# Optimization experiments

Measured on AMD Instinct MI355X. Metric: run time of the kernel, lower is better.

## Reference

```python
import jax, jax.numpy as jnp
import numpy as np

N_NODES = 50000
N_EDGES = 625000
HIDDEN = 128
N_TYPES = 4


def setup_inputs() -> dict:
    key = jax.random.key(0)
    ks = jax.random.split(key, 10)
    s = 1.0 / np.sqrt(HIDDEN)
    return {
        "node_states": jax.random.normal(ks[0], (N_NODES, HIDDEN), dtype=jnp.float32),
        "edge_index": jax.random.randint(ks[1], (2, N_EDGES), 0, N_NODES, dtype=jnp.int64),
        "edge_type": jax.random.randint(ks[2], (N_EDGES,), 0, N_TYPES, dtype=jnp.int64),
        # per-edge-type Linear(hidden, hidden): weight [T, d, d] (torch: y = x @ W.T + b)
        "edge_W": jax.random.uniform(ks[3], (N_TYPES, HIDDEN, HIDDEN), jnp.float32, -s, s),
        "edge_b": jax.random.uniform(ks[4], (N_TYPES, HIDDEN), jnp.float32, -s, s),
        # GRUCell params (torch layout: [3d, d] for r|z|n gates)
        "w_ih": jax.random.uniform(ks[5], (3 * HIDDEN, HIDDEN), jnp.float32, -s, s),
        "w_hh": jax.random.uniform(ks[6], (3 * HIDDEN, HIDDEN), jnp.float32, -s, s),
        "b_ih": jax.random.uniform(ks[7], (3 * HIDDEN,), jnp.float32, -s, s),
        "b_hh": jax.random.uniform(ks[8], (3 * HIDDEN,), jnp.float32, -s, s),
    }


def reference(node_states, edge_index, edge_type, edge_W, edge_b, w_ih, w_hh, b_ih, b_hh):
    num_nodes = node_states.shape[0]
    src, dst = edge_index[0], edge_index[1]
    x_src = node_states[src]  # [E, d] gather of source states

    # per-edge-type linear; small fixed loop over edge types, masked accumulate
    msgs = jnp.zeros_like(x_src)
    for t in range(edge_W.shape[0]):
        m_t = x_src @ edge_W[t].T + edge_b[t]  # [E, d]
        msgs = msgs + jnp.where((edge_type == t)[:, None], m_t, 0.0)

    # scatter-sum messages into destination nodes
    agg = jax.ops.segment_sum(msgs, dst, num_segments=num_nodes)  # [N, d]

    # GRUCell(agg, node_states) — torch semantics
    gi = agg @ w_ih.T + b_ih          # [N, 3d]
    gh = node_states @ w_hh.T + b_hh  # [N, 3d]
    i_r, i_z, i_n = jnp.split(gi, 3, axis=1)
    h_r, h_z, h_n = jnp.split(gh, 3, axis=1)
    r = jax.nn.sigmoid(i_r + h_r)
    z = jax.nn.sigmoid(i_z + h_z)
    n = jnp.tanh(i_n + r * h_n)
    return (1.0 - z) * n + z * node_states
```

## Files before the change

### kernel.cpp

```cpp
#include <hip/hip_runtime.h>


typedef __attribute__((ext_vector_type(8))) short short8;
typedef __attribute__((ext_vector_type(4))) float floatx4;

#define HID 128
#define NTY 4

__device__ __forceinline__ unsigned short f2bf(float f) {
    unsigned int u = __float_as_uint(f);
    unsigned int r = (u + 0x7fffu + ((u >> 16) & 1u)) >> 16;
    return (unsigned short)r;
}
__device__ __forceinline__ float bf2f(unsigned int lo16) {
    return __uint_as_float(lo16 << 16);
}


__global__ void prep_kernel(const float* __restrict__ h, unsigned short* __restrict__ hbf,
                            const float* __restrict__ W, unsigned short* __restrict__ Wc,
                            const float* __restrict__ w_ih, const float* __restrict__ w_hh,
                            unsigned short* __restrict__ Wg, int* __restrict__ deg4,
                            int total4, int nb_cvt, int N4) {
    int b = blockIdx.x, tt = threadIdx.x;
    if (b < nb_cvt) {
        int i = b * 256 + tt;
        if (i < total4) {
            float4 v = ((const float4*)h)[i];
            uint2 o;
            o.x = (unsigned int)f2bf(v.x) | ((unsigned int)f2bf(v.y) << 16);
            o.y = (unsigned int)f2bf(v.z) | ((unsigned int)f2bf(v.w) << 16);
            ((uint2*)hbf)[i] = o;
        }
    } else if (b < nb_cvt + 256) {
        int idx = (b - nb_cvt) * 256 + tt;
        int j = idx >> 9, rem = idx & 511;
        int t = rem >> 7, k = rem & 127;
        Wc[idx] = f2bf(W[(t * HID + j) * HID + k]);
    } else if (b < nb_cvt + 768) {
        int idx = (b - nb_cvt - 256) * 256 + tt;
        int row = idx >> 8, k = idx & 255;
        int j = row >> 2, g = row & 3;
        float v = 0.0f;
        if (g == 0) v = (k < 128) ? w_ih[j * 128 + k]         : w_hh[j * 128 + (k - 128)];
        else if (g == 1) v = (k < 128) ? w_ih[(128 + j) * 128 + k] : w_hh[(128 + j) * 128 + (k - 128)];
        else if (g == 2) v = (k < 128) ? w_ih[(256 + j) * 128 + k] : 0.0f;
        else             v = (k < 128) ? 0.0f : w_hh[(256 + j) * 128 + (k - 128)];
        Wg[idx] = f2bf(v);
    } else {
        int i = (b - nb_cvt - 768) * 256 + tt;
        if (i < N4) deg4[i] = 0;
    }
}


__global__ void hist4_kernel(const int* __restrict__ dst, const int* __restrict__ ety,
                             int* __restrict__ deg4, int E) {
    int e = blockIdx.x * blockDim.x + threadIdx.x;
    if (e < E) atomicAdd(&deg4[dst[e] * 4 + ety[e]], 1);
}

__global__ void scan_blocks4_kernel(const int* __restrict__ deg, int* __restrict__ rowptr,
                                    int* __restrict__ blocksum, int N4) {
    __shared__ int s[256];
    int t = threadIdx.x;
    int base = blockIdx.x * 1024 + t * 4;
    int v0 = 0, v1 = 0, v2 = 0, v3 = 0;
    if (base + 3 < N4) {
        v0 = deg[base]; v1 = deg[base + 1]; v2 = deg[base + 2]; v3 = deg[base + 3];
    } else {
        if (base < N4) v0 = deg[base];
        if (base + 1 < N4) v1 = deg[base + 1];
        if (base + 2 < N4) v2 = deg[base + 2];
    }
    int sum = v0 + v1 + v2 + v3;
    s[t] = sum;
    __syncthreads();
#pragma unroll
    for (int off = 1; off < 256; off <<= 1) {
        int x = (t >= off) ? s[t - off] : 0;
        __syncthreads();
        s[t] += x;
        __syncthreads();
    }
    int ex = s[t] - sum;
    if (base < N4) rowptr[base] = ex;
    if (base + 1 < N4) rowptr[base + 1] = ex + v0;
    if (base + 2 < N4) rowptr[base + 2] = ex + v0 + v1;
    if (base + 3 < N4) rowptr[base + 3] = ex + v0 + v1 + v2;
    if (t == 255) blocksum[blockIdx.x] = s[255];
}

__global__ void scan_top_kernel(const int* __restrict__ blocksum, int* __restrict__ blockoff, int nb) {
    __shared__ int s[256];
    int t = threadIdx.x;
    int v = (t < nb) ? blocksum[t] : 0;
    s[t] = v;
    __syncthreads();
#pragma unroll
    for (int off = 1; off < 256; off <<= 1) {
        int x = (t >= off) ? s[t - off] : 0;
        __syncthreads();
        s[t] += x;
        __syncthreads();
    }
    if (t < nb) blockoff[t] = s[t] - v;
}

__global__ void finalize4_kernel(int* __restrict__ rowptr, const int* __restrict__ blockoff,
                                 int* __restrict__ cursor, int N4, int E) {
    int i = blockIdx.x * blockDim.x + threadIdx.x;
    if (i >= N4) return;
    int r = rowptr[i] + blockoff[i >> 10];
    rowptr[i] = r;
    cursor[i] = r;
    if (i == 0) rowptr[N4] = E;
}

__global__ void fill4_kernel(const int* __restrict__ src, const int* __restrict__ dst,
                             const int* __restrict__ ety, int* __restrict__ cursor,
                             int* __restrict__ csr, int E) {
    int e = blockIdx.x * blockDim.x + threadIdx.x;
    if (e >= E) return;
    int pos = atomicAdd(&cursor[dst[e] * 4 + ety[e]], 1);
    csr[pos] = src[e];
}


__global__ void gather_s_kernel(const int* __restrict__ rowptr4, const int* __restrict__ csr,
                                const unsigned int* __restrict__ hbu,
                                float4* __restrict__ cnt4, unsigned int* __restrict__ Su, int N) {
    int w = blockIdx.x * (blockDim.x >> 6) + (threadIdx.x >> 6);
    if (w >= N) return;
    int lane = threadIdx.x & 63;
    int b0 = rowptr4[w * 4];
    int b1 = rowptr4[w * 4 + 1];
    int b2 = rowptr4[w * 4 + 2];
    int b3 = rowptr4[w * 4 + 3];
    int b4 = rowptr4[w * 4 + 4];

    float s0 = 0.f, s1 = 0.f;
    float sn0[4], sn1[4];
    int e = b0;
#pragma unroll
    for (int t = 0; t < 4; ++t) {
        int bend = (t == 0) ? b1 : (t == 1) ? b2 : (t == 2) ? b3 : b4;
        for (; e + 8 <= bend; e += 8) {
            int p[8];
            unsigned int u[8];
#pragma unroll
            for (int i = 0; i < 8; ++i) p[i] = csr[e + i];
#pragma unroll
            for (int i = 0; i < 8; ++i) u[i] = hbu[(size_t)p[i] * 64 + lane];
#pragma unroll
            for (int i = 0; i < 8; ++i) {
                s0 += bf2f(u[i] & 0xffffu);
                s1 += bf2f(u[i] >> 16);
            }
        }
        for (; e + 4 <= bend; e += 4) {
            int p[4];
            unsigned int u[4];
#pragma unroll
            for (int i = 0; i < 4; ++i) p[i] = csr[e + i];
#pragma unroll
            for (int i = 0; i < 4; ++i) u[i] = hbu[(size_t)p[i] * 64 + lane];
#pragma unroll
            for (int i = 0; i < 4; ++i) {
                s0 += bf2f(u[i] & 0xffffu);
                s1 += bf2f(u[i] >> 16);
            }
        }
        for (; e < bend; ++e) {
            unsigned int u = hbu[(size_t)csr[e] * 64 + lane];
            s0 += bf2f(u & 0xffffu);
            s1 += bf2f(u >> 16);
        }
        sn0[t] = s0;
        sn1[t] = s1;
    }
    float p0 = 0.f, p1 = 0.f;
    size_t base = (size_t)w * 256 + lane;
#pragma unroll
    for (int t = 0; t < 4; ++t) {
        float a0 = sn0[t] - p0, a1 = sn1[t] - p1;
        p0 = sn0[t]; p1 = sn1[t];
        Su[base + t * 64] = (unsigned int)f2bf(a0) | ((unsigned int)f2bf(a1) << 16);
    }
    if (lane == 0)
        cnt4[w] = make_float4((float)(b1 - b0), (float)(b2 - b1),
                              (float)(b3 - b2), (float)(b4 - b3));
}


__global__ __launch_bounds__(256) void agg_gemm(const unsigned short* __restrict__ S,
                                                const unsigned short* __restrict__ Wc,
                                                const float4* __restrict__ cnt4,
                                                const float* __restrict__ eb,
                                                unsigned short* __restrict__ aggbf, int M) {
    __shared__ __align__(16) unsigned short Ss[128][136];
    const int tid = threadIdx.x;
    const int m0 = blockIdx.x * 128;
    const int lane = tid & 63, wave = tid >> 6;
    const int wm = wave >> 1, wn = wave & 1;
    const int lm = lane & 15, quad = lane >> 4;

    floatx4 acc[4][4];
#pragma unroll
    for (int a = 0; a < 4; ++a)
#pragma unroll
        for (int b = 0; b < 4; ++b) acc[a][b] = (floatx4){0.f, 0.f, 0.f, 0.f};

    for (int c = 0; c < 4; ++c) {
        {
            int rr = tid >> 4;
            int cc = (tid & 15) * 8;
#pragma unroll
            for (int p = 0; p < 8; ++p) {
                int r = rr + p * 16;
                int gm = m0 + r;
                uint4 v = {0u, 0u, 0u, 0u};
                if (gm < M) v = *(const uint4*)(S + (size_t)gm * 512 + c * 128 + cc);
                *(uint4*)&Ss[r][cc] = v;
            }
        }
        __syncthreads();
#pragma unroll
        for (int s = 0; s < 4; ++s) {
            short8 af[4], bfr[4];
#pragma unroll
            for (int mi = 0; mi < 4; ++mi)
                af[mi] = *(const short8*)&Ss[wm * 64 + mi * 16 + lm][s * 32 + quad * 8];
#pragma unroll
            for (int ni = 0; ni < 4; ++ni) {
                int j = wn * 64 + ni * 16 + lm;
                bfr[ni] = *(const short8*)(Wc + (size_t)j * 512 + c * 128 + s * 32 + quad * 8);
            }
#pragma unroll
            for (int mi = 0; mi < 4; ++mi)
#pragma unroll
                for (int ni = 0; ni < 4; ++ni)
                    acc[mi][ni] = __builtin_amdgcn_mfma_f32_16x16x32_bf16(af[mi], bfr[ni], acc[mi][ni], 0, 0, 0);
        }
        __syncthreads();
    }
#pragma unroll
    for (int mi = 0; mi < 4; ++mi) {
        int row_b = wm * 64 + mi * 16 + quad * 4;
#pragma unroll
        for (int r = 0; r < 4; ++r) {
            int lrow = row_b + r;
            int node = m0 + lrow;
            float4 c4 = (node < M) ? cnt4[node] : make_float4(0.f, 0.f, 0.f, 0.f);
#pragma unroll
            for (int ni = 0; ni < 4; ++ni) {
                int j = wn * 64 + ni * 16 + lm;
                float v = acc[mi][ni][r];
                v += c4.x * eb[j] + c4.y * eb[HID + j] + c4.z * eb[2 * HID + j] + c4.w * eb[3 * HID + j];
                Ss[lrow][j] = f2bf(v);
            }
        }
    }
    __syncthreads();
    {
        int row = tid >> 1;
        int halfc = (tid & 1) * 64;
        int node = m0 + row;
        if (node < M) {
#pragma unroll
            for (int i = 0; i < 8; ++i)
                *(uint4*)(aggbf + (size_t)node * HID + halfc + i * 8) = *(const uint4*)&Ss[row][halfc + i * 8];
        }
    }
}


__global__ __launch_bounds__(256) void gemm_gru(const unsigned short* __restrict__ Wg,
                                                const unsigned short* __restrict__ aggbf,
                                                const unsigned short* __restrict__ hbf,
                                                const float* __restrict__ b_ih,
                                                const float* __restrict__ b_hh,
                                                float* __restrict__ out, int M) {
    __shared__ __align__(16) unsigned short Xs[64][136];
    __shared__ __align__(16) float Outs[64][68];
    const int tid = threadIdx.x;
    const int n0 = blockIdx.x * 64;
    const int gh = blockIdx.y;
    const int lane = tid & 63, w = tid >> 6;
    const int lm = lane & 15, quad = lane >> 4;

    floatx4 acc[4][4];
#pragma unroll
    for (int a = 0; a < 4; ++a)
#pragma unroll
        for (int b = 0; b < 4; ++b) acc[a][b] = (floatx4){0.f, 0.f, 0.f, 0.f};

    for (int c = 0; c < 2; ++c) {
        const unsigned short* Xp = c ? hbf : aggbf;
        {
            int rr = tid >> 4;
            int cc = (tid & 15) * 8;
#pragma unroll
            for (int p = 0; p < 4; ++p) {
                int r = rr + p * 16;
                int gn = n0 + r;
                uint4 v = {0u, 0u, 0u, 0u};
                if (gn < M) v = *(const uint4*)(Xp + (size_t)gn * HID + cc);
                *(uint4*)&Xs[r][cc] = v;
            }
        }
        __syncthreads();
#pragma unroll
        for (int s = 0; s < 4; ++s) {
            short8 bfr[4];
#pragma unroll
            for (int ni = 0; ni < 4; ++ni)
                bfr[ni] = *(const short8*)&Xs[ni * 16 + lm][s * 32 + quad * 8];
            short8 af[4];
#pragma unroll
            for (int mi = 0; mi < 4; ++mi) {
                int rowg = gh * 256 + w * 64 + mi * 16 + lm;
                af[mi] = *(const short8*)(Wg + (size_t)rowg * 256 + c * 128 + s * 32 + quad * 8);
            }
#pragma unroll
            for (int mi = 0; mi < 4; ++mi)
#pragma unroll
                for (int ni = 0; ni < 4; ++ni)
                    acc[mi][ni] = __builtin_amdgcn_mfma_f32_16x16x32_bf16(af[mi], bfr[ni], acc[mi][ni], 0, 0, 0);
        }
        __syncthreads();
    }

#pragma unroll
    for (int mi = 0; mi < 4; ++mi) {
        int jl = w * 16 + mi * 4 + quad;
        int j = gh * 64 + jl;
        float brj = b_ih[j] + b_hh[j];
        float bzj = b_ih[128 + j] + b_hh[128 + j];
        float bin = b_ih[256 + j];
        float bhn = b_hh[256 + j];
#pragma unroll
        for (int ni = 0; ni < 4; ++ni) {
            int lrow = ni * 16 + lm;
            float g0 = acc[mi][ni][0], g1 = acc[mi][ni][1];
            float g2 = acc[mi][ni][2], g3 = acc[mi][ni][3];
            float r = 1.0f / (1.0f + __expf(-(g0 + brj)));
            float z = 1.0f / (1.0f + __expf(-(g1 + bzj)));
            float nn = tanhf(g2 + bin + r * (g3 + bhn));
            float hv = bf2f((unsigned int)Xs[lrow][j]);
            Outs[lrow][jl] = (1.0f - z) * nn + z * hv;
        }
    }
    __syncthreads();
    {
        int row = tid >> 2;
        int c0 = (tid & 3) * 16;
        int node = n0 + row;
        if (node < M) {
            float* dstp = out + (size_t)node * HID + gh * 64 + c0;
#pragma unroll
            for (int i = 0; i < 4; ++i)
                *(float4*)(dstp + i * 4) = *(const float4*)&Outs[row][c0 + i * 4];
        }
    }
}


extern "C" void kernel_launch(void* const* d_in, const int* in_sizes, int n_in,
                              void* d_out, int out_size, void* d_ws, size_t ws_size,
                              hipStream_t stream) {
    const float* node_states = (const float*)d_in[0];
    const int*   edge_index  = (const int*)d_in[1];
    const int*   edge_type   = (const int*)d_in[2];
    const float* edge_W      = (const float*)d_in[3];
    const float* edge_b      = (const float*)d_in[4];
    const float* w_ih        = (const float*)d_in[5];
    const float* w_hh        = (const float*)d_in[6];
    const float* b_ih        = (const float*)d_in[7];
    const float* b_hh        = (const float*)d_in[8];

    const int M = in_sizes[0] / HID;
    const int E = in_sizes[1] / 2;
    const int N4 = M * 4;
    const int* src = edge_index;
    const int* dst = edge_index + E;

    char* ws = (char*)d_ws;
    size_t off = 0;
    unsigned short* hbf   = (unsigned short*)(ws + off); off += (size_t)M * HID * 2;
    unsigned short* aggbf = (unsigned short*)(ws + off); off += (size_t)M * HID * 2;
    unsigned short* S     = (unsigned short*)(ws + off); off += (size_t)M * 512 * 2;
    unsigned short* Wcat  = (unsigned short*)(ws + off); off += (size_t)128 * 512 * 2;
    unsigned short* Wgru  = (unsigned short*)(ws + off); off += (size_t)512 * 256 * 2;
    float*          cnt4  = (float*)(ws + off);          off += (size_t)M * 4 * 4;
    int* deg4     = (int*)(ws + off); off += (size_t)N4 * 4;
    int* rowptr4  = (int*)(ws + off); off += (size_t)(N4 + 1) * 4;
    int* cursor4  = (int*)(ws + off); off += (size_t)N4 * 4;
    int* blocksum = (int*)(ws + off); off += 256 * 4;
    int* blockoff = (int*)(ws + off); off += 256 * 4;
    int* csr      = (int*)(ws + off); off += (size_t)E * 4;

    const int total4 = M * HID / 4;
    const int nb_cvt = (total4 + 255) / 256;
    const int nb_zero = (N4 + 255) / 256;
    const int nb_scan = (N4 + 1023) / 1024;

    prep_kernel<<<nb_cvt + 768 + nb_zero, 256, 0, stream>>>(
        node_states, hbf, edge_W, Wcat, w_ih, w_hh, Wgru, deg4, total4, nb_cvt, N4);

    hist4_kernel<<<(E + 255) / 256, 256, 0, stream>>>(dst, edge_type, deg4, E);
    scan_blocks4_kernel<<<nb_scan, 256, 0, stream>>>(deg4, rowptr4, blocksum, N4);
    scan_top_kernel<<<1, 256, 0, stream>>>(blocksum, blockoff, nb_scan);
    finalize4_kernel<<<(N4 + 255) / 256, 256, 0, stream>>>(rowptr4, blockoff, cursor4, N4, E);
    fill4_kernel<<<(E + 255) / 256, 256, 0, stream>>>(src, dst, edge_type, cursor4, csr, E);

    gather_s_kernel<<<(M + 3) / 4, 256, 0, stream>>>(rowptr4, csr, (const unsigned int*)hbf,
                                                     (float4*)cnt4, (unsigned int*)S, M);

    agg_gemm<<<(M + 127) / 128, 256, 0, stream>>>(S, Wcat, (const float4*)cnt4, edge_b, aggbf, M);

    dim3 ggrid((M + 63) / 64, 2);
    gemm_gru<<<ggrid, 256, 0, stream>>>(Wgru, aggbf, hbf, b_ih, b_hh, (float*)d_out, M);
}
```

Baseline: 288.0 us.

## Fuse aggregation GEMM and GRU GEMM into one kernel keeping agg in LDS

Merges agg_gemm and gemm_gru into a single 512-thread kernel that computes the per-type aggregation for a 64-node tile, writes the bf16 result into shared memory next to the hidden states, and then runs the GRU GEMM and gate math from that buffer. This removes the aggbf round trip through global memory and one kernel launch. It also precomputes combined GRU biases in prep_kernel and uses hardware reciprocal plus an exp-based tanh. In exchange the tile shrinks, more LDS is used per block, and each block repeats the weight loads.

```diff
diff --git a/kernel.cpp b/kernel.cpp
--- a/kernel.cpp
+++ b/kernel.cpp
@@ -15,13 +15,15 @@
 __device__ __forceinline__ float bf2f(unsigned int lo16) {
     return __uint_as_float(lo16 << 16);
 }
+__device__ __forceinline__ float frcp(float x) { return __builtin_amdgcn_rcpf(x); }
 
 
 __global__ void prep_kernel(const float* __restrict__ h, unsigned short* __restrict__ hbf,
                             const float* __restrict__ W, unsigned short* __restrict__ Wc,
                             const float* __restrict__ w_ih, const float* __restrict__ w_hh,
-                            unsigned short* __restrict__ Wg, int* __restrict__ deg4,
-                            int total4, int nb_cvt, int N4) {
+                            unsigned short* __restrict__ Wg, float* __restrict__ bias4,
+                            const float* __restrict__ b_ih, const float* __restrict__ b_hh,
+                            int* __restrict__ deg4, int total4, int nb_cvt, int N4) {
     int b = blockIdx.x, tt = threadIdx.x;
     if (b < nb_cvt) {
         int i = b * 256 + tt;
@@ -47,8 +49,17 @@
         else if (g == 2) v = (k < 128) ? w_ih[(256 + j) * 128 + k] : 0.0f;
         else             v = (k < 128) ? 0.0f : w_hh[(256 + j) * 128 + (k - 128)];
         Wg[idx] = f2bf(v);
+    } else if (b == nb_cvt + 768) {
+        if (tt < 128) {
+            float4 v;
+            v.x = b_ih[tt] + b_hh[tt];
+            v.y = b_ih[128 + tt] + b_hh[128 + tt];
+            v.z = b_ih[256 + tt];
+            v.w = b_hh[256 + tt];
+            ((float4*)bias4)[tt] = v;
+        }
     } else {
-        int i = (b - nb_cvt - 768) * 256 + tt;
+        int i = (b - nb_cvt - 769) * 256 + tt;
         if (i < N4) deg4[i] = 0;
     }
 }
@@ -193,171 +204,135 @@
 }
 
 
-__global__ __launch_bounds__(256) void agg_gemm(const unsigned short* __restrict__ S,
-                                                const unsigned short* __restrict__ Wc,
-                                                const float4* __restrict__ cnt4,
-                                                const float* __restrict__ eb,
-                                                unsigned short* __restrict__ aggbf, int M) {
-    __shared__ __align__(16) unsigned short Ss[128][136];
+__global__ __launch_bounds__(512, 4) void agg_gru(const unsigned short* __restrict__ S,
+                                                  const unsigned short* __restrict__ Wc,
+                                                  const unsigned short* __restrict__ Wg,
+                                                  const unsigned short* __restrict__ hbf,
+                                                  const float4* __restrict__ cnt4,
+                                                  const float* __restrict__ eb,
+                                                  const float4* __restrict__ bias4,
+                                                  float* __restrict__ out, int M) {
+    __shared__ __align__(16) unsigned char smem[51200];
+    unsigned short (*Ss)[136] = (unsigned short (*)[136])smem;
+    unsigned short (*Xs)[264] = (unsigned short (*)[264])(smem + 17408);
+    float (*Outs)[132] = (float (*)[132])smem;
+
     const int tid = threadIdx.x;
-    const int m0 = blockIdx.x * 128;
-    const int lane = tid & 63, wave = tid >> 6;
-    const int wm = wave >> 1, wn = wave & 1;
+    const int m0 = blockIdx.x * 64;
+    const int lane = tid & 63, w = tid >> 6;
     const int lm = lane & 15, quad = lane >> 4;
 
-    floatx4 acc[4][4];
+#pragma unroll
+    for (int p = 0; p < 2; ++p) {
+        int li = p * 512 + tid;
+        int row = li >> 4, col8 = (li & 15) * 8;
+        int gm = m0 + row;
+        uint4 v = {0u, 0u, 0u, 0u};
+        if (gm < M) v = *(const uint4*)(hbf + (size_t)gm * HID + col8);
+        *(uint4*)&Xs[row][128 + col8] = v;
+    }
+
+    floatx4 accA[4];
+#pragma unroll
+    for (int a = 0; a < 4; ++a) accA[a] = (floatx4){0.f, 0.f, 0.f, 0.f};
+
+    for (int c = 0; c < 4; ++c) {
+#pragma unroll
+        for (int p = 0; p < 2; ++p) {
+            int li = p * 512 + tid;
+            int row = li >> 4, col8 = (li & 15) * 8;
+            int gm = m0 + row;
+            uint4 v = {0u, 0u, 0u, 0u};
+            if (gm < M) v = *(const uint4*)(S + (size_t)gm * 512 + c * 128 + col8);
+            *(uint4*)&Ss[row][col8] = v;
+        }
+        __syncthreads();
+#pragma unroll
+        for (int s = 0; s < 4; ++s) {
+            short8 bw = *(const short8*)(Wc + (size_t)(w * 16 + lm) * 512 + c * 128 + s * 32 + quad * 8);
+#pragma unroll
+            for (int mi = 0; mi < 4; ++mi) {
+                short8 av = *(const short8*)&Ss[mi * 16 + lm][s * 32 + quad * 8];
+                accA[mi] = __builtin_amdgcn_mfma_f32_16x16x32_bf16(av, bw, accA[mi], 0, 0, 0);
+            }
+        }
+        __syncthreads();
+    }
+
+    {
+        int j = w * 16 + lm;
+        float e0 = eb[j], e1 = eb[HID + j], e2 = eb[2 * HID + j], e3 = eb[3 * HID + j];
+#pragma unroll
+        for (int mi = 0; mi < 4; ++mi) {
+#pragma unroll
+            for (int r = 0; r < 4; ++r) {
+                int nl = mi * 16 + quad * 4 + r;
+                int gn = m0 + nl;
+                float4 c4 = (gn < M) ? cnt4[gn] : make_float4(0.f, 0.f, 0.f, 0.f);
+                float v = accA[mi][r] + c4.x * e0 + c4.y * e1 + c4.z * e2 + c4.w * e3;
+                Xs[nl][j] = f2bf(v);
+            }
+        }
+    }
+    __syncthreads();
+
+    floatx4 accB[4][4];
 #pragma unroll
     for (int a = 0; a < 4; ++a)
 #pragma unroll
-        for (int b = 0; b < 4; ++b) acc[a][b] = (floatx4){0.f, 0.f, 0.f, 0.f};
-
-    for (int c = 0; c < 4; ++c) {
-        {
-            int rr = tid >> 4;
-            int cc = (tid & 15) * 8;
-#pragma unroll
-            for (int p = 0; p < 8; ++p) {
-                int r = rr + p * 16;
-                int gm = m0 + r;
-                uint4 v = {0u, 0u, 0u, 0u};
-                if (gm < M) v = *(const uint4*)(S + (size_t)gm * 512 + c * 128 + cc);
-                *(uint4*)&Ss[r][cc] = v;
-            }
-        }
-        __syncthreads();
-#pragma unroll
-        for (int s = 0; s < 4; ++s) {
-            short8 af[4], bfr[4];
-#pragma unroll
-            for (int mi = 0; mi < 4; ++mi)
-                af[mi] = *(const short8*)&Ss[wm * 64 + mi * 16 + lm][s * 32 + quad * 8];
-#pragma unroll
-            for (int ni = 0; ni < 4; ++ni) {
-                int j = wn * 64 + ni * 16 + lm;
-                bfr[ni] = *(const short8*)(Wc + (size_t)j * 512 + c * 128 + s * 32 + quad * 8);
-            }
-#pragma unroll
-            for (int mi = 0; mi < 4; ++mi)
-#pragma unroll
-                for (int ni = 0; ni < 4; ++ni)
-                    acc[mi][ni] = __builtin_amdgcn_mfma_f32_16x16x32_bf16(af[mi], bfr[ni], acc[mi][ni], 0, 0, 0);
-        }
-        __syncthreads();
-    }
+        for (int b = 0; b < 4; ++b) accB[a][b] = (floatx4){0.f, 0.f, 0.f, 0.f};
+
+#pragma unroll
+    for (int ss = 0; ss < 8; ++ss) {
+        short8 bfr[4];
+#pragma unroll
+        for (int ni = 0; ni < 4; ++ni)
+            bfr[ni] = *(const short8*)&Xs[ni * 16 + lm][ss * 32 + quad * 8];
+        short8 af[4];
+#pragma unroll
+        for (int mi = 0; mi < 4; ++mi)
+            af[mi] = *(const short8*)(Wg + (size_t)(w * 64 + mi * 16 + lm) * 256 + ss * 32 + quad * 8);
+#pragma unroll
+        for (int mi = 0; mi < 4; ++mi)
+#pragma unroll
+            for (int ni = 0; ni < 4; ++ni)
+                accB[mi][ni] = __builtin_amdgcn_mfma_f32_16x16x32_bf16(af[mi], bfr[ni], accB[mi][ni], 0, 0, 0);
+    }
+
 #pragma unroll
     for (int mi = 0; mi < 4; ++mi) {
-        int row_b = wm * 64 + mi * 16 + quad * 4;
-#pragma unroll
-        for (int r = 0; r < 4; ++r) {
-            int lrow = row_b + r;
-            int node = m0 + lrow;
-            float4 c4 = (node < M) ? cnt4[node] : make_float4(0.f, 0.f, 0.f, 0.f);
-#pragma unroll
-            for (int ni = 0; ni < 4; ++ni) {
-                int j = wn * 64 + ni * 16 + lm;
-                float v = acc[mi][ni][r];
-                v += c4.x * eb[j] + c4.y * eb[HID + j] + c4.z * eb[2 * HID + j] + c4.w * eb[3 * HID + j];
-                Ss[lrow][j] = f2bf(v);
-            }
-        }
-    }
-    __syncthreads();
+        int j = w * 16 + mi * 4 + quad;
+        float4 bb = bias4[j];
+#pragma unroll
+        for (int ni = 0; ni < 4; ++ni) {
+            int nl = ni * 16 + lm;
+            float g0 = accB[mi][ni][0], g1 = accB[mi][ni][1];
+            float g2 = accB[mi][ni][2], g3 = accB[mi][ni][3];
+            float rr = frcp(1.f + __expf(-(g0 + bb.x)));
+            float zz = frcp(1.f + __expf(-(g1 + bb.y)));
+            float aa = g2 + bb.z + rr * (g3 + bb.w);
+            float nn = 1.f - 2.f * frcp(1.f + __expf(2.f * aa));
+            float hv = bf2f((unsigned int)Xs[nl][128 + j]);
+            accB[mi][ni][0] = nn + zz * (hv - nn);
+        }
+    }
+    __syncthreads();
+
+#pragma unroll
+    for (int mi = 0; mi < 4; ++mi) {
+        int j = w * 16 + mi * 4 + quad;
+#pragma unroll
+        for (int ni = 0; ni < 4; ++ni)
+            Outs[ni * 16 + lm][j] = accB[mi][ni][0];
+    }
+    __syncthreads();
+
     {
-        int row = tid >> 1;
-        int halfc = (tid & 1) * 64;
+        int row = tid >> 3;
+        int c0 = (tid & 7) * 16;
         int node = m0 + row;
         if (node < M) {
-#pragma unroll
-            for (int i = 0; i < 8; ++i)
-                *(uint4*)(aggbf + (size_t)node * HID + halfc + i * 8) = *(const uint4*)&Ss[row][halfc + i * 8];
-        }
-    }
-}
-
-
-__global__ __launch_bounds__(256) void gemm_gru(const unsigned short* __restrict__ Wg,
-                                                const unsigned short* __restrict__ aggbf,
-                                                const unsigned short* __restrict__ hbf,
-                                                const float* __restrict__ b_ih,
-                                                const float* __restrict__ b_hh,
-                                                float* __restrict__ out, int M) {
-    __shared__ __align__(16) unsigned short Xs[64][136];
-    __shared__ __align__(16) float Outs[64][68];
-    const int tid = threadIdx.x;
-    const int n0 = blockIdx.x * 64;
-    const int gh = blockIdx.y;
-    const int lane = tid & 63, w = tid >> 6;
-    const int lm = lane & 15, quad = lane >> 4;
-
-    floatx4 acc[4][4];
-#pragma unroll
-    for (int a = 0; a < 4; ++a)
-#pragma unroll
-        for (int b = 0; b < 4; ++b) acc[a][b] = (floatx4){0.f, 0.f, 0.f, 0.f};
-
-    for (int c = 0; c < 2; ++c) {
-        const unsigned short* Xp = c ? hbf : aggbf;
-        {
-            int rr = tid >> 4;
-            int cc = (tid & 15) * 8;
-#pragma unroll
-            for (int p = 0; p < 4; ++p) {
-                int r = rr + p * 16;
-                int gn = n0 + r;
-                uint4 v = {0u, 0u, 0u, 0u};
-                if (gn < M) v = *(const uint4*)(Xp + (size_t)gn * HID + cc);
-                *(uint4*)&Xs[r][cc] = v;
-            }
-        }
-        __syncthreads();
-#pragma unroll
-        for (int s = 0; s < 4; ++s) {
-            short8 bfr[4];
-#pragma unroll
-            for (int ni = 0; ni < 4; ++ni)
-                bfr[ni] = *(const short8*)&Xs[ni * 16 + lm][s * 32 + quad * 8];
-            short8 af[4];
-#pragma unroll
-            for (int mi = 0; mi < 4; ++mi) {
-                int rowg = gh * 256 + w * 64 + mi * 16 + lm;
-                af[mi] = *(const short8*)(Wg + (size_t)rowg * 256 + c * 128 + s * 32 + quad * 8);
-            }
-#pragma unroll
-            for (int mi = 0; mi < 4; ++mi)
-#pragma unroll
-                for (int ni = 0; ni < 4; ++ni)
-                    acc[mi][ni] = __builtin_amdgcn_mfma_f32_16x16x32_bf16(af[mi], bfr[ni], acc[mi][ni], 0, 0, 0);
-        }
-        __syncthreads();
-    }
-
-#pragma unroll
-    for (int mi = 0; mi < 4; ++mi) {
-        int jl = w * 16 + mi * 4 + quad;
-        int j = gh * 64 + jl;
-        float brj = b_ih[j] + b_hh[j];
-        float bzj = b_ih[128 + j] + b_hh[128 + j];
-        float bin = b_ih[256 + j];
-        float bhn = b_hh[256 + j];
-#pragma unroll
-        for (int ni = 0; ni < 4; ++ni) {
-            int lrow = ni * 16 + lm;
-            float g0 = acc[mi][ni][0], g1 = acc[mi][ni][1];
-            float g2 = acc[mi][ni][2], g3 = acc[mi][ni][3];
-            float r = 1.0f / (1.0f + __expf(-(g0 + brj)));
-            float z = 1.0f / (1.0f + __expf(-(g1 + bzj)));
-            float nn = tanhf(g2 + bin + r * (g3 + bhn));
-            float hv = bf2f((unsigned int)Xs[lrow][j]);
-            Outs[lrow][jl] = (1.0f - z) * nn + z * hv;
-        }
-    }
-    __syncthreads();
-    {
-        int row = tid >> 2;
-        int c0 = (tid & 3) * 16;
-        int node = n0 + row;
-        if (node < M) {
-            float* dstp = out + (size_t)node * HID + gh * 64 + c0;
+            float* dstp = out + (size_t)node * HID + c0;
 #pragma unroll
             for (int i = 0; i < 4; ++i)
                 *(float4*)(dstp + i * 4) = *(const float4*)&Outs[row][c0 + i * 4];
@@ -388,7 +363,7 @@
     char* ws = (char*)d_ws;
     size_t off = 0;
     unsigned short* hbf   = (unsigned short*)(ws + off); off += (size_t)M * HID * 2;
-    unsigned short* aggbf = (unsigned short*)(ws + off); off += (size_t)M * HID * 2;
+    float*          bias4 = (float*)(ws + off);          off += (size_t)128 * 4 * 4;
     unsigned short* S     = (unsigned short*)(ws + off); off += (size_t)M * 512 * 2;
     unsigned short* Wcat  = (unsigned short*)(ws + off); off += (size_t)128 * 512 * 2;
     unsigned short* Wgru  = (unsigned short*)(ws + off); off += (size_t)512 * 256 * 2;
@@ -405,8 +380,9 @@
     const int nb_zero = (N4 + 255) / 256;
     const int nb_scan = (N4 + 1023) / 1024;
 
-    prep_kernel<<<nb_cvt + 768 + nb_zero, 256, 0, stream>>>(
-        node_states, hbf, edge_W, Wcat, w_ih, w_hh, Wgru, deg4, total4, nb_cvt, N4);
+    prep_kernel<<<nb_cvt + 769 + nb_zero, 256, 0, stream>>>(
+        node_states, hbf, edge_W, Wcat, w_ih, w_hh, Wgru, bias4, b_ih, b_hh,
+        deg4, total4, nb_cvt, N4);
 
     hist4_kernel<<<(E + 255) / 256, 256, 0, stream>>>(dst, edge_type, deg4, E);
     scan_blocks4_kernel<<<nb_scan, 256, 0, stream>>>(deg4, rowptr4, blocksum, N4);
@@ -417,8 +393,6 @@
     gather_s_kernel<<<(M + 3) / 4, 256, 0, stream>>>(rowptr4, csr, (const unsigned int*)hbf,
                                                      (float4*)cnt4, (unsigned int*)S, M);
 
-    agg_gemm<<<(M + 127) / 128, 256, 0, stream>>>(S, Wcat, (const float4*)cnt4, edge_b, aggbf, M);
-
-    dim3 ggrid((M + 63) / 64, 2);
-    gemm_gru<<<ggrid, 256, 0, stream>>>(Wgru, aggbf, hbf, b_ih, b_hh, (float*)d_out, M);
-}
+    agg_gru<<<(M + 63) / 64, 512, 0, stream>>>(S, Wcat, Wgru, hbf, (const float4*)cnt4,
+                                               edge_b, (const float4*)bias4, (float*)d_out, M);
+}
```

Result: no change. 283.3 us (-1.6%).
